# Performance work log

Hardware: AMD Instinct MI355X
Metric: run time of the kernel (lower is better)

The kernel has to match this reference:

```python
import jax, jax.numpy as jnp
import numpy as np

B = 2048
ENB = 16      # enb_cnt (beams)
RBG = 32      # rbg_cnt
MAXREQ = 50   # max_req
OBS_F = 400   # Requests features = 50*8
H = 1024
OUT = ENB * RBG * (MAXREQ + 1)  # 26112
IN = OBS_F + ENB * RBG + ENB * MAXREQ  # 1712


def _linear_init(key, fan_in, fan_out):
    kw, kb = jax.random.split(key)
    lim = 1.0 / np.sqrt(fan_in)
    W = jax.random.uniform(kw, (fan_in, fan_out), jnp.float32, -lim, lim)
    b = jax.random.uniform(kb, (fan_out,), jnp.float32, -lim, lim)
    return W, b


def setup_inputs() -> dict:
    key = jax.random.key(0)
    ks = jax.random.split(key, 6)
    obs = jax.random.normal(ks[0], (B, OBS_F), jnp.float32)
    rbgMap = jax.random.randint(ks[1], (B, ENB, RBG), 0, 2).astype(jnp.float32)
    invFlag = (jax.random.randint(ks[2], (B, ENB, MAXREQ), 0, 3) - 1).astype(jnp.float32)
    W1, b1 = _linear_init(ks[3], IN, H)
    W2, b2 = _linear_init(ks[4], H, H)
    W3, b3 = _linear_init(ks[5], H, OUT)
    return {"obs": obs, "rbgMap": rbgMap, "invFlag": invFlag,
            "W1": W1, "b1": b1, "W2": W2, "b2": b2, "W3": W3, "b3": b3}


def reference(obs, rbgMap, invFlag, W1, b1, W2, b2, W3, b3):
    Bt = obs.shape[0]
    rbg_flat = rbgMap.reshape(Bt, ENB * RBG)                      # [B, E*R]
    inv = invFlag.reshape(Bt, ENB, MAXREQ)
    # am1: invFlag broadcast per-rbg -> [B, E*R, MAXREQ]
    am1 = jnp.broadcast_to(inv[:, :, None, :], (Bt, ENB, RBG, MAXREQ)).reshape(Bt, ENB * RBG, MAXREQ)
    rbg_exp = rbg_flat[:, :, None]                                 # [B, E*R, 1]
    # vectorized form of the nested loops:
    #   where am1 == -1: -> 1 if rbg==0, 0 if rbg==1; else unchanged
    am1 = jnp.where(am1 == -1.0, jnp.where(rbg_exp == 0.0, 1.0, 0.0), am1)
    # prepend never-masked no-op action column, mask = nonzero
    amask = jnp.concatenate([jnp.zeros((Bt, ENB * RBG, 1), am1.dtype), am1], axis=2) != 0
    # dense MLP on concatenated observation
    inp = jnp.concatenate([obs, rbg_flat, invFlag.reshape(Bt, -1)], axis=1)  # [B, 1712]
    h = jnp.tanh(inp @ W1 + b1)
    h = jnp.tanh(h @ W2 + b2)
    logits = (h @ W3 + b3).reshape(Bt, ENB * RBG, MAXREQ + 1)
    logits = jnp.where(amask, -jnp.inf, logits)
    return logits
```

## Files before the change

kernel.cpp:

```cpp
#include <hip/hip_runtime.h>
#include <math.h>

#define B_    2048
#define OBSF_ 400
#define H_    1024
#define IN_   1712
#define INP_  1728
#define KS1_  54
#define KSH_  32
#define OUT_  26112
#define NCOL_ 51
#define MAXQ_ 50

#define NEG_BIG (-3.0e38f)

typedef __attribute__((ext_vector_type(4))) float  floatx4;
typedef __bf16 bf16x8 __attribute__((ext_vector_type(8)));

__device__ __forceinline__ unsigned short f2b(float v) {
    unsigned u = __float_as_uint(v);
    u += 0x7FFFu + ((u >> 16) & 1u);
    return (unsigned short)(u >> 16);
}


__global__ __launch_bounds__(256)
void pack_frag(const float* __restrict__ obs,
               const float* __restrict__ rbg,
               const float* __restrict__ inv,
               unsigned short* __restrict__ P) {
    const int tid = threadIdx.x;
    const int wave = tid >> 6, lane = tid & 63;
    const int cid = blockIdx.x * 4 + wave;
    const int ks = cid % KS1_, r16 = cid / KS1_;
    const int r = r16 * 16 + (lane & 15);
    const int kb = ks * 32 + (lane >> 4) * 8;
    __attribute__((aligned(16))) unsigned short tmp[8];
    #pragma unroll
    for (int j = 0; j < 8; j++) {
        int k = kb + j;
        float v = 0.0f;
        if (k < OBSF_)            v = obs[r * OBSF_ + k];
        else if (k < OBSF_ + 512) v = rbg[r * 512 + (k - OBSF_)];
        else if (k < IN_)         v = inv[r * 800 + (k - OBSF_ - 512)];
        tmp[j] = f2b(v);
    }
    *(uint4*)(P + ((size_t)(r16 * KS1_ + ks) * 64 + lane) * 8) = *(const uint4*)tmp;
}

__global__ __launch_bounds__(256)
void transpose_frag(const float* __restrict__ W, unsigned short* __restrict__ P,
                    int K, int N, int KS) {
    __shared__ float tile[32][129];
    const int n0 = blockIdx.x * 128, k0 = blockIdx.y * 32;
    const int tid = threadIdx.x;
    const int nn = tid & 127, kk0 = tid >> 7;
    #pragma unroll
    for (int i = 0; i < 16; i++) {
        int k = k0 + kk0 + i * 2;
        float v = 0.0f;
        if (k < K) v = W[(size_t)k * N + n0 + nn];
        tile[kk0 + i * 2][nn] = v;
    }
    __syncthreads();
    const int wave = tid >> 6, lane = tid & 63;
    const int i16 = lane & 15, q = lane >> 4;
    #pragma unroll
    for (int c2 = 0; c2 < 2; c2++) {
        const int c = wave * 2 + c2;
        __attribute__((aligned(16))) unsigned short tmp[8];
        #pragma unroll
        for (int j = 0; j < 8; j++) tmp[j] = f2b(tile[q * 8 + j][c * 16 + i16]);
        *(uint4*)(P + ((size_t)(((n0 >> 4) + c) * KS + (k0 >> 5)) * 64 + lane) * 8) =
            *(const uint4*)tmp;
    }
}

template<int MT, int NT, int KS, int EPI>
__global__ __launch_bounds__(256, 2)
void gemm_frag(const unsigned short* __restrict__ Ap,
               const unsigned short* __restrict__ Bp,
               const float* __restrict__ bias,
               void* __restrict__ outv,
               const float* __restrict__ rbg,
               const float* __restrict__ inv,
               int KSo) {
    const int tid = threadIdx.x;
    const int wave = tid >> 6, lane = tid & 63;
    const int wtm = blockIdx.y * 2 + (wave >> 1);
    const int wtn = blockIdx.x * 2 + (wave & 1);
    const int m16base = wtm * MT, n16base = wtn * NT;

    const unsigned short* pa = Ap + (size_t)m16base * KS * 512 + lane * 8;
    const unsigned short* pb = Bp + (size_t)n16base * KS * 512 + lane * 8;

    floatx4 acc[MT][NT];
    #pragma unroll
    for (int i = 0; i < MT; i++)
        #pragma unroll
        for (int j = 0; j < NT; j++) acc[i][j] = (floatx4){0.f, 0.f, 0.f, 0.f};

    bf16x8 a0[MT], b0[NT], a1[MT], b1[NT];
    #define LOADA(dst, ks_)                                                    \
        _Pragma("unroll") for (int mt = 0; mt < MT; mt++)                      \
            dst[mt] = *(const bf16x8*)(pa + (size_t)mt * KS * 512 + (ks_) * 512);
    #define LOADB(dst, ks_)                                                    \
        _Pragma("unroll") for (int nt = 0; nt < NT; nt++)                      \
            dst[nt] = *(const bf16x8*)(pb + (size_t)nt * KS * 512 + (ks_) * 512);
    #define MFMA(aa, bb)                                                       \
        _Pragma("unroll") for (int mt = 0; mt < MT; mt++)                      \
            _Pragma("unroll") for (int nt = 0; nt < NT; nt++)                  \
                acc[mt][nt] = __builtin_amdgcn_mfma_f32_16x16x32_bf16(         \
                    aa[mt], bb[nt], acc[mt][nt], 0, 0, 0);

    LOADA(a0, 0); LOADB(b0, 0);
    for (int ks = 0; ks < KS; ks += 2) {
        LOADA(a1, ks + 1); LOADB(b1, ks + 1);
        MFMA(a0, b0);
        int k2 = (ks + 2 < KS) ? ks + 2 : 0;
        LOADA(a0, k2); LOADB(b0, k2);
        MFMA(a1, b1);
    }
    #undef LOADA
    #undef LOADB
    #undef MFMA

    const int quad = lane >> 4;
    #pragma unroll
    for (int nt = 0; nt < NT; nt++) {
        const int col = (n16base + nt) * 16 + (lane & 15);
        const float bv = bias[col];
        unsigned short* Hp = (unsigned short*)outv;
        const int ko = col >> 5, kb = (col >> 3) & 3, kj = col & 7;
        #pragma unroll
        for (int mt = 0; mt < MT; mt++) {
            const int m16 = m16base + mt;
            #pragma unroll
            for (int r = 0; r < 4; r++) {
                const int mlo = quad * 4 + r;
                Hp[((size_t)(m16 * KSo + ko) * 64 + (mlo | (kb << 4))) * 8 + kj] =
                    f2b(tanhf(acc[mt][nt][r] + bv));
            }
        }
    }
}

typedef __attribute__((address_space(1))) const unsigned int gu32;
typedef __attribute__((address_space(3))) unsigned int su32;
__device__ __forceinline__ void async_copy16(unsigned short* l, const unsigned short* g) {
    __builtin_amdgcn_global_load_lds((gu32*)g, (su32*)l, 16, 0, 0);
}

template<int MT, int NT, int KS>
__global__ __launch_bounds__(256, 3)
void gemm_lds(const unsigned short* __restrict__ Ap,
              const unsigned short* __restrict__ Bp,
              const float* __restrict__ bias,
              float* __restrict__ C,
              const float* __restrict__ rbg,
              const float* __restrict__ inv) {
    constexpr int ACH = 2 * MT;
    constexpr int CPW = ACH / 4;
    static_assert(CPW == 2 && NT == 4, "vmcnt literals assume 2 stage + 4 B loads");
    static_assert(KS % 6 == 2, "prologue 2 + 6k main + tail 2");
    __shared__ __align__(16) unsigned short lds[3][ACH][512];

    const int tid  = threadIdx.x;
    const int wave = tid >> 6, lane = tid & 63;

    const int i = blockIdx.x;
    const int xcd = i & 7, j = i >> 3;
    const int g = xcd * 408 + j;
    const int panel = g >> 4;
    const int m     = g & 15;
    const int blk_m16 = m * ACH;
    const int blk_n16 = panel * 2 * NT;

    const int rg = wave >> 1, cg = wave & 1;
    const int m16base = blk_m16 + rg * MT;
    const int n16base = blk_n16 + cg * NT;

    const unsigned short* ga[CPW];
    #pragma unroll
    for (int q = 0; q < CPW; q++)
        ga[q] = Ap + (size_t)(blk_m16 + wave * CPW + q) * KS * 512 + lane * 8;
    const unsigned short* pb[NT];
    #pragma unroll
    for (int nt = 0; nt < NT; nt++)
        pb[nt] = Bp + (size_t)(n16base + nt) * KS * 512 + lane * 8;

    floatx4 acc[MT][NT];
    #pragma unroll
    for (int a = 0; a < MT; a++)
        #pragma unroll
        for (int b = 0; b < NT; b++) acc[a][b] = (floatx4){0.f, 0.f, 0.f, 0.f};

    bf16x8 bb0[NT], bb1[NT];

    #define STAGE(bufi, ksv) do {                                              \
        _Pragma("unroll")                                                      \
        for (int q = 0; q < CPW; q++)                                          \
            async_copy16(&lds[bufi][wave * CPW + q][0],                        \
                         ga[q] + (size_t)(ksv) * 512);                         \
    } while (0)

    #define LOADB(dst, ksv) do {                                               \
        _Pragma("unroll")                                                      \
        for (int nt = 0; nt < NT; nt++)                                        \
            dst[nt] = *(const bf16x8*)(pb[nt] + (size_t)(ksv) * 512);          \
    } while (0)

    #define COMPUTE(p3, B) do {                                                \
        bf16x8 af[MT];                                                         \
        _Pragma("unroll")                                                      \
        for (int mt = 0; mt < MT; mt++)                                        \
            af[mt] = *(const bf16x8*)&lds[p3][rg * MT + mt][lane * 8];         \
        __builtin_amdgcn_s_setprio(1);                                         \
        _Pragma("unroll")                                                      \
        for (int mt = 0; mt < MT; mt++)                                        \
            _Pragma("unroll")                                                  \
            for (int nt = 0; nt < NT; nt++)                                    \
                acc[mt][nt] = __builtin_amdgcn_mfma_f32_16x16x32_bf16(         \
                    af[mt], B[nt], acc[mt][nt], 0, 0, 0);                      \
        __builtin_amdgcn_s_setprio(0);                                         \
    } while (0)

    #define STEP(P3, NB3, BCUR, BNXT, tv) do {                                 \
        STAGE(NB3, (tv) + 2);                                                  \
        LOADB(BNXT, (tv) + 1);                                                 \
        COMPUTE(P3, BCUR);                                                     \
        asm volatile("s_waitcnt vmcnt(6)" ::: "memory");                       \
        __builtin_amdgcn_s_barrier();                                          \
        asm volatile("" ::: "memory");                                         \
    } while (0)

    STAGE(0, 0);
    STAGE(1, 1);
    LOADB(bb0, 0);
    LOADB(bb1, 1);
    asm volatile("s_waitcnt vmcnt(10)" ::: "memory");
    __builtin_amdgcn_s_barrier();
    asm volatile("" ::: "memory");

    #pragma unroll 1
    for (int t = 0; t < KS - 2; t += 6) {
        STEP(0, 2, bb0, bb1, t);
        STEP(1, 0, bb1, bb0, t + 1);
        STEP(2, 1, bb0, bb1, t + 2);
        STEP(0, 2, bb1, bb0, t + 3);
        STEP(1, 0, bb0, bb1, t + 4);
        STEP(2, 1, bb1, bb0, t + 5);
    }
    LOADB(bb1, KS - 1);
    COMPUTE(0, bb0);
    asm volatile("s_waitcnt vmcnt(4)" ::: "memory");
    __builtin_amdgcn_s_barrier();
    asm volatile("" ::: "memory");
    COMPUTE(1, bb1);
    #undef STEP
    #undef STAGE
    #undef LOADB
    #undef COMPUTE

    const int quad = lane >> 4;
    #pragma unroll
    for (int nt = 0; nt < NT; nt++) {
        const int col = (n16base + nt) * 16 + (lane & 15);
        const float bvs = bias[col];
        const int jj = col / NCOL_;
        const int qq = col - jj * NCOL_;
        const int e  = jj >> 5;
        #pragma unroll
        for (int mt = 0; mt < MT; mt++) {
            const int row0 = (m16base + mt) * 16 + quad * 4;
            #pragma unroll
            for (int r = 0; r < 4; r++) {
                const int row = row0 + r;
                float v = acc[mt][nt][r] + bvs;
                if (qq > 0) {
                    float iv = inv[(size_t)row * 800 + e * MAXQ_ + (qq - 1)];
                    if (iv == 1.0f ||
                        (iv == -1.0f && rbg[(size_t)row * 512 + jj] == 0.0f))
                        v = NEG_BIG;
                }
                __builtin_nontemporal_store(v, &C[(size_t)row * OUT_ + col]);
            }
        }
    }
}

extern "C" void kernel_launch(void* const* d_in, const int* in_sizes, int n_in,
                              void* d_out, int out_size, void* d_ws, size_t ws_size,
                              hipStream_t stream) {
    const float* obs = (const float*)d_in[0];
    const float* rbg = (const float*)d_in[1];
    const float* inv = (const float*)d_in[2];
    const float* W1  = (const float*)d_in[3];
    const float* b1  = (const float*)d_in[4];
    const float* W2  = (const float*)d_in[5];
    const float* b2  = (const float*)d_in[6];
    const float* W3  = (const float*)d_in[7];
    const float* b3  = (const float*)d_in[8];
    float* out = (float*)d_out;

    char* ws = (char*)d_ws;
    unsigned short* inpP = (unsigned short*)ws;  ws += (size_t)B_ * INP_ * 2;
    unsigned short* W1P  = (unsigned short*)ws;  ws += (size_t)H_ * INP_ * 2;
    unsigned short* W2P  = (unsigned short*)ws;  ws += (size_t)H_ * H_ * 2;
    unsigned short* W3P  = (unsigned short*)ws;  ws += (size_t)OUT_ * H_ * 2;
    unsigned short* h1P  = (unsigned short*)ws;  ws += (size_t)B_ * H_ * 2;
    unsigned short* h2P  = (unsigned short*)ws;

    pack_frag<<<dim3(KS1_ * (B_ / 16) / 4), 256, 0, stream>>>(obs, rbg, inv, inpP);

    transpose_frag<<<dim3(H_ / 128, INP_ / 32), 256, 0, stream>>>(W1, W1P, IN_, H_, KS1_);
    transpose_frag<<<dim3(H_ / 128, H_ / 32),   256, 0, stream>>>(W2, W2P, H_, H_, KSH_);
    transpose_frag<<<dim3(OUT_ / 128, H_ / 32), 256, 0, stream>>>(W3, W3P, H_, OUT_, KSH_);

    gemm_frag<2, 2, KS1_, 0><<<dim3(H_ / 64, B_ / 64), 256, 0, stream>>>(
        inpP, W1P, b1, h1P, nullptr, nullptr, KSH_);
    gemm_frag<2, 2, KSH_, 0><<<dim3(H_ / 64, B_ / 64), 256, 0, stream>>>(
        h1P, W2P, b2, h2P, nullptr, nullptr, KSH_);
    gemm_lds<4, 4, KSH_><<<dim3(16 * (OUT_ / 128)), 256, 0, stream>>>(
        h2P, W3P, b3, out, rbg, inv);
}
```

Before: 597.5 us.

## Deepen B-operand register prefetch to two steps and vectorize weight transpose loads

The LDS GEMM now keeps three B-fragment register buffers and loads B two k-steps ahead instead of one. The vmcnt wait threshold is raised to match, and the main loop period drops from six to three steps. This is meant to hide more global-load latency for the B operand, at the cost of extra VGPRs, which could hurt occupancy at launch bounds of 3. Separately, the weight transpose kernel reads float4 vectors per thread instead of scalars, to cut the number of load instructions.

Result: faster. 573.3 us (-4.1%).

```diff
diff --git a/kernel.cpp b/kernel.cpp
--- a/kernel.cpp
+++ b/kernel.cpp
@@ -54,13 +54,17 @@
     __shared__ float tile[32][129];
     const int n0 = blockIdx.x * 128, k0 = blockIdx.y * 32;
     const int tid = threadIdx.x;
-    const int nn = tid & 127, kk0 = tid >> 7;
-    #pragma unroll
-    for (int i = 0; i < 16; i++) {
-        int k = k0 + kk0 + i * 2;
-        float v = 0.0f;
-        if (k < K) v = W[(size_t)k * N + n0 + nn];
-        tile[kk0 + i * 2][nn] = v;
+    #pragma unroll
+    for (int pz = 0; pz < 4; pz++) {
+        const int idx = pz * 256 + tid;
+        const int row = idx >> 5, c4 = (idx & 31) * 4;
+        const int k = k0 + row;
+        floatx4 v = (floatx4){0.f, 0.f, 0.f, 0.f};
+        if (k < K) v = *(const floatx4*)&W[(size_t)k * N + n0 + c4];
+        tile[row][c4 + 0] = v[0];
+        tile[row][c4 + 1] = v[1];
+        tile[row][c4 + 2] = v[2];
+        tile[row][c4 + 3] = v[3];
     }
     __syncthreads();
     const int wave = tid >> 6, lane = tid & 63;
@@ -162,7 +166,7 @@
     constexpr int ACH = 2 * MT;
     constexpr int CPW = ACH / 4;
     static_assert(CPW == 2 && NT == 4, "vmcnt literals assume 2 stage + 4 B loads");
-    static_assert(KS % 6 == 2, "prologue 2 + 6k main + tail 2");
+    static_assert((KS - 2) % 3 == 0, "main loop is period-3");
     __shared__ __align__(16) unsigned short lds[3][ACH][512];
 
     const int tid  = threadIdx.x;
@@ -195,7 +199,7 @@
         #pragma unroll
         for (int b = 0; b < NT; b++) acc[a][b] = (floatx4){0.f, 0.f, 0.f, 0.f};
 
-    bf16x8 bb0[NT], bb1[NT];
+    bf16x8 bb0[NT], bb1[NT], bb2[NT];
 
     #define STAGE(bufi, ksv) do {                                              \
         _Pragma("unroll")                                                      \
@@ -225,11 +229,11 @@
         __builtin_amdgcn_s_setprio(0);                                         \
     } while (0)
 
-    #define STEP(P3, NB3, BCUR, BNXT, tv) do {                                 \
+    #define STEP(P3, NB3, BC, BN, tv) do {                                     \
         STAGE(NB3, (tv) + 2);                                                  \
-        LOADB(BNXT, (tv) + 1);                                                 \
-        COMPUTE(P3, BCUR);                                                     \
-        asm volatile("s_waitcnt vmcnt(6)" ::: "memory");                       \
+        LOADB(BN, (tv) + 2);                                                   \
+        COMPUTE(P3, BC);                                                       \
+        asm volatile("s_waitcnt vmcnt(10)" ::: "memory");                      \
         __builtin_amdgcn_s_barrier();                                          \
         asm volatile("" ::: "memory");                                         \
     } while (0)
@@ -243,15 +247,11 @@
     asm volatile("" ::: "memory");
 
     #pragma unroll 1
-    for (int t = 0; t < KS - 2; t += 6) {
-        STEP(0, 2, bb0, bb1, t);
+    for (int t = 0; t < KS - 2; t += 3) {
+        STEP(0, 2, bb0, bb2, t);
         STEP(1, 0, bb1, bb0, t + 1);
-        STEP(2, 1, bb0, bb1, t + 2);
-        STEP(0, 2, bb1, bb0, t + 3);
-        STEP(1, 0, bb0, bb1, t + 4);
-        STEP(2, 1, bb1, bb0, t + 5);
-    }
-    LOADB(bb1, KS - 1);
+        STEP(2, 1, bb2, bb1, t + 2);
+    }
     COMPUTE(0, bb0);
     asm volatile("s_waitcnt vmcnt(4)" ::: "memory");
     __builtin_amdgcn_s_barrier();
```
